# Kernel tuning notes

Hardware: AMD Instinct MI355X
Metric: run time of the kernel (lower is better)

Reference implementation:

```python
import jax, jax.numpy as jnp
import numpy as np

D_MODEL = 1024
N_HEADS = 16
D_K = D_MODEL // N_HEADS


def setup_inputs() -> dict:
    key = jax.random.key(0)
    ks = jax.random.split(key, 9)
    s = 1.0 / np.sqrt(D_MODEL)
    x = jax.random.normal(ks[0], (2, 2048, D_MODEL), dtype=jnp.float32)
    Wq = jax.random.normal(ks[1], (D_MODEL, D_MODEL), dtype=jnp.float32) * s
    bq = jnp.zeros((D_MODEL,), jnp.float32)
    Wk = jax.random.normal(ks[2], (D_MODEL, D_MODEL), dtype=jnp.float32) * s
    bk = jnp.zeros((D_MODEL,), jnp.float32)
    Wv = jax.random.normal(ks[3], (D_MODEL, D_MODEL), dtype=jnp.float32) * s
    bv = jnp.zeros((D_MODEL,), jnp.float32)
    Wo = jax.random.normal(ks[4], (D_MODEL, D_MODEL), dtype=jnp.float32) * s
    bo = jnp.zeros((D_MODEL,), jnp.float32)
    return {"x": x, "Wq": Wq, "bq": bq, "Wk": Wk, "bk": bk,
            "Wv": Wv, "bv": bv, "Wo": Wo, "bo": bo}


def reference(x, Wq, bq, Wk, bk, Wv, bv, Wo, bo):
    B, T, C = x.shape
    H, Dk = N_HEADS, D_K
    # QKV projections, reshape to [B, H, T, Dk]
    q = (x @ Wq + bq).reshape(B, T, H, Dk).transpose(0, 2, 1, 3)
    k = (x @ Wk + bk).reshape(B, T, H, Dk).transpose(0, 2, 1, 3)
    v = (x @ Wv + bv).reshape(B, T, H, Dk).transpose(0, 2, 1, 3)
    scale = 1.0 / np.sqrt(Dk).astype(np.float32)
    att = jnp.einsum('bhqd,bhkd->bhqk', q, k) * scale  # [B,H,T,T]
    causal = jnp.tril(jnp.ones((T, T), dtype=bool))
    att = jnp.where(causal, att, -jnp.inf)
    att = jax.nn.softmax(att, axis=-1)
    y = jnp.einsum('bhqk,bhkd->bhqd', att, v)  # [B,H,T,Dk]
    y = y.transpose(0, 2, 1, 3).reshape(B, T, C)
    return y @ Wo + bo
```

## Files before the change

kernel.cpp:

```cpp
#include <hip/hip_runtime.h>
#include <stdint.h>

#define D_MODEL 1024
#define N_HEADS 16
#define D_K     64
#define T_SEQ   2048
#define BATCH   2
#define M_TOT   (BATCH * T_SEQ)
#define QCH     128

typedef __attribute__((ext_vector_type(8))) short  short8;
typedef __attribute__((ext_vector_type(4))) float  f32x4;
typedef __attribute__((ext_vector_type(4))) unsigned short u16x4;

typedef __attribute__((address_space(1))) void gvoid;
typedef __attribute__((address_space(3))) void lvoid;

#define QSCALE 0.18033688011112042f

static __device__ __forceinline__ unsigned short f2bf(float f) {
    union { float f; unsigned u; } v; v.f = f;
    unsigned u = v.u;
    u += 0x7fffu + ((u >> 16) & 1u);
    return (unsigned short)(u >> 16);
}
static __device__ __forceinline__ float bf2f(unsigned short s) {
    union { unsigned u; float f; } v; v.u = ((unsigned)s) << 16;
    return v.f;
}
static __device__ __forceinline__ float fexp2(float x) {
    float r;
    asm("v_exp_f32 %0, %1" : "=v"(r) : "v"(x));
    return r;
}
static __device__ __forceinline__ unsigned cvt_pk_bf16(float lo, float hi) {
    unsigned r;
    asm("v_cvt_pk_bf16_f32 %0, %1, %2" : "=v"(r) : "v"(lo), "v"(hi));
    return r;
}

__global__ void cvt_x(const float* __restrict__ in, unsigned short* __restrict__ out) {
    int idx = blockIdx.x * blockDim.x + threadIdx.x;
    const float4* in4 = (const float4*)in;
    float4 v = in4[idx];
    u16x4 o;
    o.x = f2bf(v.x); o.y = f2bf(v.y); o.z = f2bf(v.z); o.w = f2bf(v.w);
    *(u16x4*)&out[(size_t)idx * 4] = o;
}

__global__ void cvt_w_t(const float* w0, const float* w1, const float* w2, const float* w3,
                        unsigned short* o0, unsigned short* o1, unsigned short* o2, unsigned short* o3) {
    const float* w; unsigned short* o;
    switch (blockIdx.z) {
        case 0: w = w0; o = o0; break;
        case 1: w = w1; o = o1; break;
        case 2: w = w2; o = o2; break;
        default: w = w3; o = o3; break;
    }
    __shared__ float tile[32][33];
    int n0 = blockIdx.x * 32, k0 = blockIdx.y * 32;
    int tx = threadIdx.x, ty = threadIdx.y;
    #pragma unroll
    for (int r = 0; r < 32; r += 8)
        tile[ty + r][tx] = w[(size_t)(k0 + ty + r) * D_MODEL + n0 + tx];
    __syncthreads();
    #pragma unroll
    for (int r = 0; r < 32; r += 8)
        o[(size_t)(n0 + ty + r) * D_MODEL + k0 + tx] = f2bf(tile[tx][ty + r]);
}

__global__ __launch_bounds__(256) void gemm_qkv(const unsigned short* __restrict__ A,
                                                const unsigned short* __restrict__ wq,
                                                const unsigned short* __restrict__ wk,
                                                const unsigned short* __restrict__ wv,
                                                const float* __restrict__ bq,
                                                const float* __restrict__ bk,
                                                const float* __restrict__ bv,
                                                unsigned short* __restrict__ qo,
                                                unsigned short* __restrict__ ko,
                                                unsigned short* __restrict__ vo) {
    const int z = blockIdx.z;
    const unsigned short* Bt = (z == 0) ? wq : (z == 1) ? wk : wv;
    const float* bias = (z == 0) ? bq : (z == 1) ? bk : bv;
    const float alpha = (z == 0) ? QSCALE : 1.0f;

    __shared__ unsigned short lA[128 * 32];
    __shared__ unsigned short lB[128 * 32];
    const int tid  = threadIdx.x;
    const int w    = tid >> 6, lane = tid & 63;
    const int tm   = blockIdx.y, tn = blockIdx.x;
    const int wm   = w & 1, wn = w >> 1;
    const int i16  = lane & 15, g4 = lane >> 4;
    f32x4 acc[4][4] = {};

    const int rA0 = tm * 128, rB0 = tn * 128;
    const int srow = lane >> 2;
    const int skc  = (lane & 3) * 8;

    for (int k0 = 0; k0 < D_MODEL; k0 += 32) {
        #pragma unroll
        for (int is = 0; is < 2; ++is) {
            int c   = is * 4 + w;
            int row = c * 16 + srow;
            __builtin_amdgcn_global_load_lds(
                (gvoid*)(A + (size_t)(rA0 + row) * D_MODEL + k0 + skc),
                (lvoid*)&lA[c * 512], 16, 0, 0);
            __builtin_amdgcn_global_load_lds(
                (gvoid*)(Bt + (size_t)(rB0 + row) * D_MODEL + k0 + skc),
                (lvoid*)&lB[c * 512], 16, 0, 0);
        }
        __syncthreads();
        short8 af[4], bfr[4];
        #pragma unroll
        for (int mi = 0; mi < 4; ++mi)
            af[mi] = *(const short8*)&lA[(wm * 64 + mi * 16 + i16) * 32 + g4 * 8];
        #pragma unroll
        for (int ni = 0; ni < 4; ++ni)
            bfr[ni] = *(const short8*)&lB[(wn * 64 + ni * 16 + i16) * 32 + g4 * 8];
        #pragma unroll
        for (int mi = 0; mi < 4; ++mi)
            #pragma unroll
            for (int ni = 0; ni < 4; ++ni)
                acc[mi][ni] = __builtin_amdgcn_mfma_f32_16x16x32_bf16(af[mi], bfr[ni], acc[mi][ni], 0, 0, 0);
        __syncthreads();
    }

    #pragma unroll
    for (int mi = 0; mi < 4; ++mi)
        #pragma unroll
        for (int ni = 0; ni < 4; ++ni) {
            int col = tn * 128 + wn * 64 + ni * 16 + i16;
            float bv2 = bias[col];
            #pragma unroll
            for (int r = 0; r < 4; ++r) {
                int row = tm * 128 + wm * 64 + mi * 16 + g4 * 4 + r;
                float val = (acc[mi][ni][r] + bv2) * alpha;
                int b = row >> 11, t = row & (T_SEQ - 1);
                int h = col >> 6,  d = col & (D_K - 1);
                unsigned short bfv = f2bf(val);
                if (z == 2)
                    vo[(((size_t)(b * N_HEADS + h)) * D_K + d) * T_SEQ + t] = bfv;
                else if (z == 1)
                    ko[(((size_t)(b * N_HEADS + h)) * T_SEQ + t) * D_K + d] = bfv;
                else
                    qo[(((size_t)(b * N_HEADS + h)) * T_SEQ + t) * D_K + d] = bfv;
            }
        }
}

__global__ __launch_bounds__(256) void gemm_out(const unsigned short* __restrict__ A,
                                                const unsigned short* __restrict__ Bt,
                                                const float* __restrict__ bias,
                                                float* __restrict__ Cout) {
    __shared__ unsigned short lA[128 * 32];
    __shared__ unsigned short lB[128 * 32];
    const int tid  = threadIdx.x;
    const int w    = tid >> 6, lane = tid & 63;
    const int tm   = blockIdx.y, tn = blockIdx.x;
    const int wm   = w & 1, wn = w >> 1;
    const int i16  = lane & 15, g4 = lane >> 4;
    f32x4 acc[4][4] = {};

    const int rA0 = tm * 128, rB0 = tn * 128;
    const int srow = lane >> 2;
    const int skc  = (lane & 3) * 8;

    for (int k0 = 0; k0 < D_MODEL; k0 += 32) {
        #pragma unroll
        for (int is = 0; is < 2; ++is) {
            int c   = is * 4 + w;
            int row = c * 16 + srow;
            __builtin_amdgcn_global_load_lds(
                (gvoid*)(A + (size_t)(rA0 + row) * D_MODEL + k0 + skc),
                (lvoid*)&lA[c * 512], 16, 0, 0);
            __builtin_amdgcn_global_load_lds(
                (gvoid*)(Bt + (size_t)(rB0 + row) * D_MODEL + k0 + skc),
                (lvoid*)&lB[c * 512], 16, 0, 0);
        }
        __syncthreads();
        short8 af[4], bfr[4];
        #pragma unroll
        for (int mi = 0; mi < 4; ++mi)
            af[mi] = *(const short8*)&lA[(wm * 64 + mi * 16 + i16) * 32 + g4 * 8];
        #pragma unroll
        for (int ni = 0; ni < 4; ++ni)
            bfr[ni] = *(const short8*)&lB[(wn * 64 + ni * 16 + i16) * 32 + g4 * 8];
        #pragma unroll
        for (int mi = 0; mi < 4; ++mi)
            #pragma unroll
            for (int ni = 0; ni < 4; ++ni)
                acc[mi][ni] = __builtin_amdgcn_mfma_f32_16x16x32_bf16(af[mi], bfr[ni], acc[mi][ni], 0, 0, 0);
        __syncthreads();
    }

    #pragma unroll
    for (int mi = 0; mi < 4; ++mi)
        #pragma unroll
        for (int ni = 0; ni < 4; ++ni) {
            int col = tn * 128 + wn * 64 + ni * 16 + i16;
            float bv2 = bias[col];
            #pragma unroll
            for (int r = 0; r < 4; ++r) {
                int row = tm * 128 + wm * 64 + mi * 16 + g4 * 4 + r;
                Cout[(size_t)row * D_MODEL + col] = acc[mi][ni][r] + bv2;
            }
        }
}

__global__ __launch_bounds__(256, 3) void flash6(const unsigned short* __restrict__ q,
                                                 const unsigned short* __restrict__ k,
                                                 const unsigned short* __restrict__ vt,
                                                 unsigned short* __restrict__ op01,
                                                 unsigned short* __restrict__ op2,
                                                 float* __restrict__ lws) {
    __shared__ unsigned short lK[2][64 * 64];
    __shared__ unsigned short lV[2][64 * 64];
    __shared__ unsigned short lP[4][16 * 64];
    const int tid  = threadIdx.x;
    const int w    = tid >> 6, lane = tid & 63;
    const int i16  = lane & 15, g4 = lane >> 4;
    const int l8   = lane & 7,  g8 = lane >> 3;
    const int nb   = blockIdx.x;
    const int p    = nb & 7;
    const int s    = (nb >> 3) % 3;
    const int bh   = nb / 24;

    const unsigned short* kp = k  + (size_t)bh * T_SEQ * D_K;
    const unsigned short* vp = vt + (size_t)bh * D_K * T_SEQ;
    unsigned short* Pw = &lP[w][0];
    const int swz  = (i16 & 7) << 3;
    const int csrc = (l8 ^ g8) << 3;

    const int b = bh >> 4, hh = bh & 15;
    unsigned short* op = (s == 2) ? op2 : op01 + (size_t)s * ((size_t)M_TOT * D_MODEL);

    auto stage = [&](int buf, int kv0s) {
        #pragma unroll
        for (int i = 0; i < 2; ++i) {
            const int cidx = w * 2 + i;
            const int row  = cidx * 8 + g8;
            __builtin_amdgcn_global_load_lds(
                (gvoid*)(kp + (size_t)(kv0s + row) * D_K + csrc),
                (lvoid*)&lK[buf][cidx * 512], 16, 0, 0);
            __builtin_amdgcn_global_load_lds(
                (gvoid*)(vp + (size_t)row * T_SEQ + kv0s + csrc),
                (lvoid*)&lV[buf][cidx * 512], 16, 0, 0);
        }
    };

    #pragma unroll 1
    for (int ci = 0; ci < 2; ++ci) {
        const int c   = ci ? p : (15 - p);
        const int q0w = c * QCH + w * 32;
        const int cnt = (2 * c + 1 >= s) ? (2 * c + 1 - s) / 3 + 1 : 0;

        const unsigned short* qp = q + ((size_t)bh * T_SEQ + q0w) * D_K;
        short8 qf[2][2];
        #pragma unroll
        for (int qt = 0; qt < 2; ++qt)
            #pragma unroll
            for (int ks = 0; ks < 2; ++ks)
                qf[qt][ks] = *(const short8*)&qp[(qt * 16 + i16) * D_K + ks * 32 + g4 * 8];

        f32x4 o[2][4] = {};
        float l[2] = {0.f, 0.f};

        if (cnt > 0) stage(0, s * 64);
        __syncthreads();

        for (int it = 0; it < cnt; ++it) {
            const int cur = it & 1;
            const int kv0 = (s + 3 * it) * 64;
            if (it + 1 < cnt) stage(cur ^ 1, kv0 + 192);

            if (kv0 <= q0w + 31) {
                const bool act0 = (kv0 <= q0w + 15);
                const unsigned short* Kc = &lK[cur][0];
                const unsigned short* Vc = &lV[cur][0];

                f32x4 sA[4][2] = {};
                __builtin_amdgcn_s_setprio(1);
                #pragma unroll
                for (int ks = 0; ks < 2; ++ks)
                    #pragma unroll
                    for (int kt = 0; kt < 4; ++kt) {
                        short8 ka = *(const short8*)&Kc[(kt * 16 + i16) * 64 + ((ks * 32 + g4 * 8) ^ swz)];
                        if (act0)
                            sA[kt][0] = __builtin_amdgcn_mfma_f32_16x16x32_bf16(ka, qf[0][ks], sA[kt][0], 0, 0, 0);
                        sA[kt][1] = __builtin_amdgcn_mfma_f32_16x16x32_bf16(ka, qf[1][ks], sA[kt][1], 0, 0, 0);
                    }
                __builtin_amdgcn_s_setprio(0);

                #pragma unroll
                for (int qt = 0; qt < 2; ++qt) {
                    if (qt == 0 && !act0) continue;
                    const int qrow = q0w + qt * 16 + i16;
                    const bool diag = (kv0 + 63 > q0w + qt * 16);
                    float ps = 0.f;
                    unsigned pk[8];
                    #pragma unroll
                    for (int kt = 0; kt < 4; ++kt) {
                        f32x4 sc = sA[kt][qt];
                        if (diag) {
                            #pragma unroll
                            for (int r = 0; r < 4; ++r)
                                if (kv0 + kt * 16 + g4 * 4 + r > qrow) sc[r] = -3e38f;
                        }
                        float p0 = fexp2(sc[0]), p1 = fexp2(sc[1]);
                        float p2 = fexp2(sc[2]), p3 = fexp2(sc[3]);
                        ps += (p0 + p1) + (p2 + p3);
                        pk[kt * 2]     = cvt_pk_bf16(p0, p1);
                        pk[kt * 2 + 1] = cvt_pk_bf16(p2, p3);
                    }
                    l[qt] += ps;
                    #pragma unroll
                    for (int kt = 0; kt < 4; ++kt) {
                        uint2 v2; v2.x = pk[kt * 2]; v2.y = pk[kt * 2 + 1];
                        *(uint2*)&Pw[i16 * 64 + ((kt * 16 + g4 * 4) ^ swz)] = v2;
                    }
                    short8 pB0 = *(const short8*)&Pw[i16 * 64 + (( 0 + g4 * 8) ^ swz)];
                    short8 pB1 = *(const short8*)&Pw[i16 * 64 + ((32 + g4 * 8) ^ swz)];
                    __builtin_amdgcn_s_setprio(1);
                    #pragma unroll
                    for (int dt = 0; dt < 4; ++dt) {
                        short8 va0 = *(const short8*)&Vc[(dt * 16 + i16) * 64 + (( 0 + g4 * 8) ^ swz)];
                        short8 va1 = *(const short8*)&Vc[(dt * 16 + i16) * 64 + ((32 + g4 * 8) ^ swz)];
                        o[qt][dt] = __builtin_amdgcn_mfma_f32_16x16x32_bf16(va0, pB0, o[qt][dt], 0, 0, 0);
                        o[qt][dt] = __builtin_amdgcn_mfma_f32_16x16x32_bf16(va1, pB1, o[qt][dt], 0, 0, 0);
                    }
                    __builtin_amdgcn_s_setprio(0);
                }
            }
            __syncthreads();
        }

        #pragma unroll
        for (int qt = 0; qt < 2; ++qt) {
            float lt = l[qt] + __shfl_xor(l[qt], 16);
            lt += __shfl_xor(lt, 32);
            const int trow = q0w + qt * 16 + i16;
            if (g4 == 0)
                lws[((size_t)s * 32 + bh) * T_SEQ + trow] = lt;
            #pragma unroll
            for (int dt = 0; dt < 4; ++dt) {
                u16x4 ov;
                ov.x = f2bf(o[qt][dt][0]);
                ov.y = f2bf(o[qt][dt][1]);
                ov.z = f2bf(o[qt][dt][2]);
                ov.w = f2bf(o[qt][dt][3]);
                *(u16x4*)&op[((size_t)(b * T_SEQ) + trow) * D_MODEL + hh * D_K + dt * 16 + g4 * 4] = ov;
            }
        }
        __syncthreads();
    }
}

__global__ __launch_bounds__(256) void merge3(const unsigned short* __restrict__ op01,
                                              const unsigned short* __restrict__ op2,
                                              const float* __restrict__ lws,
                                              unsigned short* __restrict__ y) {
    const int idx = blockIdx.x * 256 + threadIdx.x;
    const int gl  = idx * 8;
    const int row = gl >> 10;
    const int col = gl & 1023;
    const int b = row >> 11, t = row & (T_SEQ - 1), h = col >> 6;
    const int bh = b * 16 + h;
    const float l0 = lws[((size_t)bh) * T_SEQ + t];
    const float l1 = lws[((size_t)(32 + bh)) * T_SEQ + t];
    const float l2 = lws[((size_t)(64 + bh)) * T_SEQ + t];
    const float inv = 1.0f / (l0 + l1 + l2);
    short8 a0 = *(const short8*)&op01[gl];
    short8 a1 = *(const short8*)&op01[(size_t)M_TOT * D_MODEL + gl];
    short8 a2 = *(const short8*)&op2[gl];
    short8 r;
    #pragma unroll
    for (int j = 0; j < 8; ++j) {
        float f = bf2f((unsigned short)a0[j]) + bf2f((unsigned short)a1[j]) + bf2f((unsigned short)a2[j]);
        r[j] = (short)f2bf(f * inv);
    }
    *(short8*)&y[gl] = r;
}

extern "C" void kernel_launch(void* const* d_in, const int* in_sizes, int n_in,
                              void* d_out, int out_size, void* d_ws, size_t ws_size,
                              hipStream_t stream) {
    const float* x  = (const float*)d_in[0];
    const float* Wq = (const float*)d_in[1];
    const float* bq = (const float*)d_in[2];
    const float* Wk = (const float*)d_in[3];
    const float* bk = (const float*)d_in[4];
    const float* Wv = (const float*)d_in[5];
    const float* bv = (const float*)d_in[6];
    const float* Wo = (const float*)d_in[7];
    const float* bo = (const float*)d_in[8];

    uint8_t* ws = (uint8_t*)d_ws;
    const size_t MB = (size_t)1 << 20;
    unsigned short* xb  = (unsigned short*)(ws);
    unsigned short* wqt = (unsigned short*)(ws + 8  * MB);
    unsigned short* wkt = (unsigned short*)(ws + 10 * MB);
    unsigned short* wvt = (unsigned short*)(ws + 12 * MB);
    unsigned short* wot = (unsigned short*)(ws + 14 * MB);
    unsigned short* qb  = (unsigned short*)(ws + 16 * MB);
    unsigned short* kb  = (unsigned short*)(ws + 24 * MB);
    unsigned short* vtb = (unsigned short*)(ws + 32 * MB);
    float* lws = (float*)(ws + 8 * MB);

    cvt_x<<<4096, 256, 0, stream>>>(x, xb);
    cvt_w_t<<<dim3(32, 32, 4), dim3(32, 8), 0, stream>>>(Wq, Wk, Wv, Wo, wqt, wkt, wvt, wot);

    gemm_qkv<<<dim3(8, 32, 3), 256, 0, stream>>>(xb, wqt, wkt, wvt, bq, bk, bv, qb, kb, vtb);

    flash6<<<768, 256, 0, stream>>>(qb, kb, vtb, (unsigned short*)d_out, xb, lws);
    merge3<<<2048, 256, 0, stream>>>((const unsigned short*)d_out, xb, lws, qb);

    gemm_out<<<dim3(8, 32), 256, 0, stream>>>(qb, wot, bo, (float*)d_out);
}
```

Before: 120.8 us.

## Double GEMM K-tile to 64 with XOR-swizzled LDS and split flash P stores from PV

Both projection GEMMs now stage 64-wide K tiles instead of 32, halving the number of barrier pairs per K loop. The LDS layout gets an XOR swizzle on both the global-to-LDS write and the fragment reads to avoid bank conflicts. In the flash kernel each wave gets a separate P buffer per query tile, so both tiles' P stores happen before the PV MFMA phase and the priority raise covers one larger MFMA block. This costs twice the LDS per GEMM block and more LDS in the flash kernel, which could reduce occupancy.

```diff
diff --git a/kernel.cpp b/kernel.cpp
--- a/kernel.cpp
+++ b/kernel.cpp
@@ -84,44 +84,48 @@
     const float* bias = (z == 0) ? bq : (z == 1) ? bk : bv;
     const float alpha = (z == 0) ? QSCALE : 1.0f;
 
-    __shared__ unsigned short lA[128 * 32];
-    __shared__ unsigned short lB[128 * 32];
+    __shared__ unsigned short lA[128 * 64];
+    __shared__ unsigned short lB[128 * 64];
     const int tid  = threadIdx.x;
     const int w    = tid >> 6, lane = tid & 63;
     const int tm   = blockIdx.y, tn = blockIdx.x;
     const int wm   = w & 1, wn = w >> 1;
     const int i16  = lane & 15, g4 = lane >> 4;
+    const int l8   = lane & 7,  g8 = lane >> 3;
     f32x4 acc[4][4] = {};
 
     const int rA0 = tm * 128, rB0 = tn * 128;
-    const int srow = lane >> 2;
-    const int skc  = (lane & 3) * 8;
-
-    for (int k0 = 0; k0 < D_MODEL; k0 += 32) {
-        #pragma unroll
-        for (int is = 0; is < 2; ++is) {
+    const int scol = (l8 ^ (g8 & 7)) << 3;
+    const int rswz = (i16 & 7) << 3;
+
+    for (int k0 = 0; k0 < D_MODEL; k0 += 64) {
+        #pragma unroll
+        for (int is = 0; is < 4; ++is) {
             int c   = is * 4 + w;
-            int row = c * 16 + srow;
-            __builtin_amdgcn_global_load_lds(
-                (gvoid*)(A + (size_t)(rA0 + row) * D_MODEL + k0 + skc),
+            int row = c * 8 + g8;
+            __builtin_amdgcn_global_load_lds(
+                (gvoid*)(A + (size_t)(rA0 + row) * D_MODEL + k0 + scol),
                 (lvoid*)&lA[c * 512], 16, 0, 0);
             __builtin_amdgcn_global_load_lds(
-                (gvoid*)(Bt + (size_t)(rB0 + row) * D_MODEL + k0 + skc),
+                (gvoid*)(Bt + (size_t)(rB0 + row) * D_MODEL + k0 + scol),
                 (lvoid*)&lB[c * 512], 16, 0, 0);
         }
         __syncthreads();
-        short8 af[4], bfr[4];
-        #pragma unroll
-        for (int mi = 0; mi < 4; ++mi)
-            af[mi] = *(const short8*)&lA[(wm * 64 + mi * 16 + i16) * 32 + g4 * 8];
-        #pragma unroll
-        for (int ni = 0; ni < 4; ++ni)
-            bfr[ni] = *(const short8*)&lB[(wn * 64 + ni * 16 + i16) * 32 + g4 * 8];
-        #pragma unroll
-        for (int mi = 0; mi < 4; ++mi)
+        #pragma unroll
+        for (int ks = 0; ks < 2; ++ks) {
+            short8 af[4], bfr[4];
+            #pragma unroll
+            for (int mi = 0; mi < 4; ++mi)
+                af[mi] = *(const short8*)&lA[(wm * 64 + mi * 16 + i16) * 64 + ((ks * 32 + g4 * 8) ^ rswz)];
             #pragma unroll
             for (int ni = 0; ni < 4; ++ni)
-                acc[mi][ni] = __builtin_amdgcn_mfma_f32_16x16x32_bf16(af[mi], bfr[ni], acc[mi][ni], 0, 0, 0);
+                bfr[ni] = *(const short8*)&lB[(wn * 64 + ni * 16 + i16) * 64 + ((ks * 32 + g4 * 8) ^ rswz)];
+            #pragma unroll
+            for (int mi = 0; mi < 4; ++mi)
+                #pragma unroll
+                for (int ni = 0; ni < 4; ++ni)
+                    acc[mi][ni] = __builtin_amdgcn_mfma_f32_16x16x32_bf16(af[mi], bfr[ni], acc[mi][ni], 0, 0, 0);
+        }
         __syncthreads();
     }
 
@@ -152,44 +156,48 @@
                                                 const unsigned short* __restrict__ Bt,
                                                 const float* __restrict__ bias,
                                                 float* __restrict__ Cout) {
-    __shared__ unsigned short lA[128 * 32];
-    __shared__ unsigned short lB[128 * 32];
+    __shared__ unsigned short lA[128 * 64];
+    __shared__ unsigned short lB[128 * 64];
     const int tid  = threadIdx.x;
     const int w    = tid >> 6, lane = tid & 63;
     const int tm   = blockIdx.y, tn = blockIdx.x;
     const int wm   = w & 1, wn = w >> 1;
     const int i16  = lane & 15, g4 = lane >> 4;
+    const int l8   = lane & 7,  g8 = lane >> 3;
     f32x4 acc[4][4] = {};
 
     const int rA0 = tm * 128, rB0 = tn * 128;
-    const int srow = lane >> 2;
-    const int skc  = (lane & 3) * 8;
-
-    for (int k0 = 0; k0 < D_MODEL; k0 += 32) {
-        #pragma unroll
-        for (int is = 0; is < 2; ++is) {
+    const int scol = (l8 ^ (g8 & 7)) << 3;
+    const int rswz = (i16 & 7) << 3;
+
+    for (int k0 = 0; k0 < D_MODEL; k0 += 64) {
+        #pragma unroll
+        for (int is = 0; is < 4; ++is) {
             int c   = is * 4 + w;
-            int row = c * 16 + srow;
-            __builtin_amdgcn_global_load_lds(
-                (gvoid*)(A + (size_t)(rA0 + row) * D_MODEL + k0 + skc),
+            int row = c * 8 + g8;
+            __builtin_amdgcn_global_load_lds(
+                (gvoid*)(A + (size_t)(rA0 + row) * D_MODEL + k0 + scol),
                 (lvoid*)&lA[c * 512], 16, 0, 0);
             __builtin_amdgcn_global_load_lds(
-                (gvoid*)(Bt + (size_t)(rB0 + row) * D_MODEL + k0 + skc),
+                (gvoid*)(Bt + (size_t)(rB0 + row) * D_MODEL + k0 + scol),
                 (lvoid*)&lB[c * 512], 16, 0, 0);
         }
         __syncthreads();
-        short8 af[4], bfr[4];
-        #pragma unroll
-        for (int mi = 0; mi < 4; ++mi)
-            af[mi] = *(const short8*)&lA[(wm * 64 + mi * 16 + i16) * 32 + g4 * 8];
-        #pragma unroll
-        for (int ni = 0; ni < 4; ++ni)
-            bfr[ni] = *(const short8*)&lB[(wn * 64 + ni * 16 + i16) * 32 + g4 * 8];
-        #pragma unroll
-        for (int mi = 0; mi < 4; ++mi)
+        #pragma unroll
+        for (int ks = 0; ks < 2; ++ks) {
+            short8 af[4], bfr[4];
+            #pragma unroll
+            for (int mi = 0; mi < 4; ++mi)
+                af[mi] = *(const short8*)&lA[(wm * 64 + mi * 16 + i16) * 64 + ((ks * 32 + g4 * 8) ^ rswz)];
             #pragma unroll
             for (int ni = 0; ni < 4; ++ni)
-                acc[mi][ni] = __builtin_amdgcn_mfma_f32_16x16x32_bf16(af[mi], bfr[ni], acc[mi][ni], 0, 0, 0);
+                bfr[ni] = *(const short8*)&lB[(wn * 64 + ni * 16 + i16) * 64 + ((ks * 32 + g4 * 8) ^ rswz)];
+            #pragma unroll
+            for (int mi = 0; mi < 4; ++mi)
+                #pragma unroll
+                for (int ni = 0; ni < 4; ++ni)
+                    acc[mi][ni] = __builtin_amdgcn_mfma_f32_16x16x32_bf16(af[mi], bfr[ni], acc[mi][ni], 0, 0, 0);
+        }
         __syncthreads();
     }
 
@@ -207,7 +215,7 @@
         }
 }
 
-__global__ __launch_bounds__(256, 3) void flash6(const unsigned short* __restrict__ q,
+__global__ __launch_bounds__(256, 3) void flash7(const unsigned short* __restrict__ q,
                                                  const unsigned short* __restrict__ k,
                                                  const unsigned short* __restrict__ vt,
                                                  unsigned short* __restrict__ op01,
@@ -215,7 +223,7 @@
                                                  float* __restrict__ lws) {
     __shared__ unsigned short lK[2][64 * 64];
     __shared__ unsigned short lV[2][64 * 64];
-    __shared__ unsigned short lP[4][16 * 64];
+    __shared__ unsigned short lP[4][2][16 * 64];
     const int tid  = threadIdx.x;
     const int w    = tid >> 6, lane = tid & 63;
     const int i16  = lane & 15, g4 = lane >> 4;
@@ -227,7 +235,6 @@
 
     const unsigned short* kp = k  + (size_t)bh * T_SEQ * D_K;
     const unsigned short* vp = vt + (size_t)bh * D_K * T_SEQ;
-    unsigned short* Pw = &lP[w][0];
     const int swz  = (i16 & 7) << 3;
     const int csrc = (l8 ^ g8) << 3;
 
@@ -313,14 +320,21 @@
                         pk[kt * 2 + 1] = cvt_pk_bf16(p2, p3);
                     }
                     l[qt] += ps;
+                    unsigned short* Pw = &lP[w][qt][0];
                     #pragma unroll
                     for (int kt = 0; kt < 4; ++kt) {
                         uint2 v2; v2.x = pk[kt * 2]; v2.y = pk[kt * 2 + 1];
                         *(uint2*)&Pw[i16 * 64 + ((kt * 16 + g4 * 4) ^ swz)] = v2;
                     }
+                }
+
+                __builtin_amdgcn_s_setprio(1);
+                #pragma unroll
+                for (int qt = 0; qt < 2; ++qt) {
+                    if (qt == 0 && !act0) continue;
+                    const unsigned short* Pw = &lP[w][qt][0];
                     short8 pB0 = *(const short8*)&Pw[i16 * 64 + (( 0 + g4 * 8) ^ swz)];
                     short8 pB1 = *(const short8*)&Pw[i16 * 64 + ((32 + g4 * 8) ^ swz)];
-                    __builtin_amdgcn_s_setprio(1);
                     #pragma unroll
                     for (int dt = 0; dt < 4; ++dt) {
                         short8 va0 = *(const short8*)&Vc[(dt * 16 + i16) * 64 + (( 0 + g4 * 8) ^ swz)];
@@ -328,8 +342,8 @@
                         o[qt][dt] = __builtin_amdgcn_mfma_f32_16x16x32_bf16(va0, pB0, o[qt][dt], 0, 0, 0);
                         o[qt][dt] = __builtin_amdgcn_mfma_f32_16x16x32_bf16(va1, pB1, o[qt][dt], 0, 0, 0);
                     }
-                    __builtin_amdgcn_s_setprio(0);
                 }
+                __builtin_amdgcn_s_setprio(0);
             }
             __syncthreads();
         }
@@ -411,7 +425,7 @@
 
     gemm_qkv<<<dim3(8, 32, 3), 256, 0, stream>>>(xb, wqt, wkt, wvt, bq, bk, bv, qb, kb, vtb);
 
-    flash6<<<768, 256, 0, stream>>>(qb, kb, vtb, (unsigned short*)d_out, xb, lws);
+    flash7<<<768, 256, 0, stream>>>(qb, kb, vtb, (unsigned short*)d_out, xb, lws);
     merge3<<<2048, 256, 0, stream>>>((const unsigned short*)d_out, xb, lws, qb);
 
     gemm_out<<<dim3(8, 32), 256, 0, stream>>>(qb, wot, bo, (float*)d_out);
```

After: 139.6 us. 15.6% more time.
